# Performance work log

Hardware: AMD Instinct MI355X
Metric: run time of the kernel (lower is better)

Reference implementation:

```python
import jax, jax.numpy as jnp
import numpy as np

NUM_GRAPHS = 256
EPS = 1e-5
SLOPE = 0.01

def _lrelu(x):
    return jnp.where(x >= 0, x, SLOPE * x)

def _gcn(x, W, b, src, dst, ew, n_nodes):
    # GCNConv(normalize=False): out[dst] = sum_e ew[e] * (x @ W)[src[e]] + b
    h = x @ W
    msg = h[src] * ew[:, None]
    agg = jax.ops.segment_sum(msg, dst, num_segments=n_nodes)
    return agg + b

def _bn(x, g, beta):
    # training-mode BatchNorm1d over node dim, biased variance
    m = jnp.mean(x, axis=0)
    v = jnp.mean((x - m) ** 2, axis=0)
    return (x - m) * jax.lax.rsqrt(v + EPS) * g + beta

def setup_inputs() -> dict:
    key = jax.random.key(0)
    ks = jax.random.split(key, 20)
    N, E, F0 = 20000, 320000, 1280
    dims = [(F0, 640), (640, 512), (512, 256), (256, 256)]
    inp = {
        'x': jax.random.normal(ks[0], (N, F0), dtype=jnp.float32),
        'edge_index': jax.random.randint(ks[1], (2, E), 0, N, dtype=jnp.int64),
        'edge_weigth': jax.random.uniform(ks[2], (E,), dtype=jnp.float32),
        'batch': jnp.sort(jax.random.randint(ks[3], (N,), 0, NUM_GRAPHS, dtype=jnp.int64)),
    }
    for i, (fi, fo) in enumerate(dims, start=1):
        inp[f'W{i}'] = jax.random.normal(ks[3 + i], (fi, fo), dtype=jnp.float32) * (1.0 / np.sqrt(fi))
        inp[f'b{i}'] = jnp.zeros((fo,), dtype=jnp.float32)
        inp[f'g{i}'] = jnp.ones((fo,), dtype=jnp.float32)
        inp[f'be{i}'] = jnp.zeros((fo,), dtype=jnp.float32)
    fdims = [(256, 128), (128, 64), (64, 2)]
    for i, (fi, fo) in enumerate(fdims, start=1):
        inp[f'Wf{i}'] = jax.random.normal(ks[10 + i], (fi, fo), dtype=jnp.float32) * np.sqrt(2.0 / (fi + fo))
        inp[f'bf{i}'] = jnp.zeros((fo,), dtype=jnp.float32)
    return inp

def reference(x, edge_index, edge_weigth, batch,
              W1, b1, g1, be1, W2, b2, g2, be2,
              W3, b3, g3, be3, W4, b4, g4, be4,
              Wf1, bf1, Wf2, bf2, Wf3, bf3):
    n = x.shape[0]
    src, dst = edge_index[0], edge_index[1]
    h = _lrelu(_bn(_gcn(x, W1, b1, src, dst, edge_weigth, n), g1, be1))
    h = _lrelu(_bn(_gcn(h, W2, b2, src, dst, edge_weigth, n), g2, be2))
    h = _lrelu(_bn(_gcn(h, W3, b3, src, dst, edge_weigth, n), g3, be3))
    h = _lrelu(_bn(_gcn(h, W4, b4, src, dst, edge_weigth, n), g4, be4))
    pooled = jax.ops.segment_sum(h, batch, num_segments=NUM_GRAPHS)  # [G, 256]
    out = _lrelu(pooled @ Wf1 + bf1)
    out = _lrelu(out @ Wf2 + bf2)
    out = _lrelu(out @ Wf3 + bf3)
    return out
```

## Files before the change

kernel.cpp:

```cpp
#include <hip/hip_runtime.h>

typedef short bf16x8 __attribute__((ext_vector_type(8)));
typedef float f32x4  __attribute__((ext_vector_type(4)));

__device__ __forceinline__ float bf2f(unsigned short h){
  union { unsigned int u; float f; } c; c.u = ((unsigned int)h) << 16; return c.f;
}
__device__ __forceinline__ unsigned short f2bf(float f){
  union { float f; unsigned int u; } c; c.f = f;
  unsigned int u = c.u;
  return (unsigned short)((u + 0x7fffu + ((u >> 16) & 1u)) >> 16);
}
__device__ __forceinline__ void gload_lds16(const void* g, void* l){
  __builtin_amdgcn_global_load_lds((const __attribute__((address_space(1))) unsigned int*)g,
                                   (__attribute__((address_space(3))) unsigned int*)l, 16, 0, 0);
}
__device__ __forceinline__ float lrelu(float x){ return x >= 0.f ? x : 0.01f * x; }

__global__ void cvt_f32_bf16(const float* __restrict__ x, unsigned short* __restrict__ o, int n4){
  int i = blockIdx.x * 256 + threadIdx.x;
  if (i >= n4) return;
  float4 v = ((const float4*)x)[i];
  ushort4 r; r.x = f2bf(v.x); r.y = f2bf(v.y); r.z = f2bf(v.z); r.w = f2bf(v.w);
  ((ushort4*)o)[i] = r;
}

__global__ void wt_kernel(const float* __restrict__ Wm, unsigned short* __restrict__ Wt, int K, int Nf){
  __shared__ float tile[32][33];
  int n0 = blockIdx.x * 32, k0 = blockIdx.y * 32;
  int tx = threadIdx.x, ty = threadIdx.y;
  for (int i = ty; i < 32; i += 8)
    tile[i][tx] = Wm[(size_t)(k0 + i) * Nf + n0 + tx];
  __syncthreads();
  for (int i = ty; i < 32; i += 8)
    Wt[(size_t)(n0 + i) * K + k0 + tx] = f2bf(tile[tx][i]);
}

__global__ void hist_kernel(const int* __restrict__ dst, int* __restrict__ hist, int E){
  int e = blockIdx.x * 256 + threadIdx.x;
  if (e < E) atomicAdd(&hist[dst[e]], 1);
}

__global__ void scan_kernel(int* __restrict__ hist, int* __restrict__ cursor, int n, int total){
  __shared__ int partials[1024];
  const int CH = 20;
  int t = threadIdx.x;
  int base = t * CH;
  int local[CH];
  int s = 0;
  for (int i = 0; i < CH; i++){
    int idx = base + i;
    int v = (idx < n) ? hist[idx] : 0;
    local[i] = s; s += v;
  }
  partials[t] = s;
  __syncthreads();
  for (int off = 1; off < 1024; off <<= 1){
    int v = (t >= off) ? partials[t - off] : 0;
    __syncthreads();
    if (t >= off) partials[t] += v;
    __syncthreads();
  }
  int pre = (t == 0) ? 0 : partials[t - 1];
  for (int i = 0; i < CH; i++){
    int idx = base + i;
    if (idx < n){ int v = pre + local[i]; hist[idx] = v; cursor[idx] = v; }
  }
  if (t == 0){ hist[n] = total; }
}

__global__ void scatter_kernel(const int* __restrict__ src, const int* __restrict__ dst,
                               const float* __restrict__ ew, int* __restrict__ cursor,
                               int* __restrict__ so, float* __restrict__ eo, int E){
  int e = blockIdx.x * 256 + threadIdx.x;
  if (e >= E) return;
  int d = dst[e];
  int p = atomicAdd(&cursor[d], 1);
  so[p] = src[e]; eo[p] = ew[e];
}

__global__ __launch_bounds__(256) void gemm_bf16(const unsigned short* __restrict__ A,
                                                 const unsigned short* __restrict__ Bt,
                                                 unsigned short* __restrict__ C,
                                                 int Nf, int K, int Nt){
  __shared__ unsigned short lsA[128 * 64];
  __shared__ unsigned short lsB[128 * 64];
  const int nwg = gridDim.x;
  const int orig = blockIdx.x;
  const int q = nwg >> 3, r = nwg & 7;
  const int xcd = orig & 7, idx = orig >> 3;
  const int wgid = (xcd < r ? xcd * (q + 1) : r * (q + 1) + (xcd - r) * q) + idx;
  const int mt = wgid / Nt, nt = wgid % Nt;

  const int tid = threadIdx.x;
  const int wave = tid >> 6, lane = tid & 63;
  const int wr = wave >> 1, wc = wave & 1;
  const size_t tm = (size_t)mt * 128, tn = (size_t)nt * 128;

  f32x4 acc[4][4] = {};

  const int lrow = lane >> 3;
  const int lcol = (lane & 7) * 8;
  const unsigned short* Ab = A  + (tm + wave * 32 + lrow) * (size_t)K + lcol;
  const unsigned short* Bb = Bt + (tn + wave * 32 + lrow) * (size_t)K + lcol;
  unsigned short* lA0 = &lsA[(wave * 32) * 64];
  unsigned short* lB0 = &lsB[(wave * 32) * 64];

  for (int k0 = 0; k0 < K; k0 += 64){
    #pragma unroll
    for (int s = 0; s < 4; s++){
      gload_lds16(Ab + (size_t)s * 8 * K + k0, lA0 + s * 8 * 64);
      gload_lds16(Bb + (size_t)s * 8 * K + k0, lB0 + s * 8 * 64);
    }
    __syncthreads();
    #pragma unroll
    for (int kk = 0; kk < 2; kk++){
      bf16x8 af[4], bfr[4];
      #pragma unroll
      for (int m = 0; m < 4; m++)
        af[m] = *(const bf16x8*)&lsA[(wr * 64 + m * 16 + (lane & 15)) * 64 + kk * 32 + (lane >> 4) * 8];
      #pragma unroll
      for (int n = 0; n < 4; n++)
        bfr[n] = *(const bf16x8*)&lsB[(wc * 64 + n * 16 + (lane & 15)) * 64 + kk * 32 + (lane >> 4) * 8];
      #pragma unroll
      for (int m = 0; m < 4; m++)
        #pragma unroll
        for (int n = 0; n < 4; n++)
          acc[m][n] = __builtin_amdgcn_mfma_f32_16x16x32_bf16(af[m], bfr[n], acc[m][n], 0, 0, 0);
    }
    __syncthreads();
  }
  #pragma unroll
  for (int m = 0; m < 4; m++)
    #pragma unroll
    for (int n = 0; n < 4; n++)
      #pragma unroll
      for (int j = 0; j < 4; j++){
        size_t row = tm + wr * 64 + m * 16 + (lane >> 4) * 4 + j;
        size_t col = tn + wc * 64 + n * 16 + (lane & 15);
        C[row * Nf + col] = f2bf(acc[m][n][j]);
      }
}

template<int F, int C, int G, int NPB>
__global__ __launch_bounds__(C * G * NPB)
void agg_panel(const unsigned short* __restrict__ H,
               const int* __restrict__ rp,
               const int* __restrict__ srcs,
               const float* __restrict__ ews,
               float* __restrict__ AGG, int Nnodes){
  const int flat = blockIdx.x;
  const int panel = flat & 7;
  const int ngrp = flat >> 3;
  const int t = threadIdx.x;
  const int c = t % C;
  const int g = (t / C) % G;
  const int ni = t / (C * G);
  const int node = ngrp * NPB + ni;
  const bool valid = (node < Nnodes);
  const size_t coff = (size_t)panel * (C * 8) + (size_t)c * 8;

  int e0 = 0, e1 = 0;
  if (valid){ e0 = rp[node]; e1 = rp[node + 1]; }

  float acc[8] = {0.f,0.f,0.f,0.f,0.f,0.f,0.f,0.f};
  int e = e0 + g;
  for (; e + G < e1; e += 2 * G){
    int s0 = srcs[e];     float w0 = ews[e];
    int s1 = srcs[e + G]; float w1 = ews[e + G];
    bf16x8 v0 = *(const bf16x8*)&H[(size_t)s0 * F + coff];
    bf16x8 v1 = *(const bf16x8*)&H[(size_t)s1 * F + coff];
    #pragma unroll
    for (int j = 0; j < 8; j++) acc[j] += w0 * bf2f((unsigned short)v0[j]);
    #pragma unroll
    for (int j = 0; j < 8; j++) acc[j] += w1 * bf2f((unsigned short)v1[j]);
  }
  if (e < e1){
    int s0 = srcs[e]; float w0 = ews[e];
    bf16x8 v0 = *(const bf16x8*)&H[(size_t)s0 * F + coff];
    #pragma unroll
    for (int j = 0; j < 8; j++) acc[j] += w0 * bf2f((unsigned short)v0[j]);
  }

  __shared__ float red[NPB * G * C * 8];
  if (g > 0){
    #pragma unroll
    for (int j = 0; j < 8; j++) red[((ni * G + g) * C + c) * 8 + j] = acc[j];
  }
  __syncthreads();
  if (g == 0 && valid){
    #pragma unroll
    for (int gg = 1; gg < G; gg++)
      #pragma unroll
      for (int j = 0; j < 8; j++) acc[j] += red[((ni * G + gg) * C + c) * 8 + j];
    float* orow = AGG + (size_t)node * F + coff;
    *(float4*)(orow)     = *(float4*)&acc[0];
    *(float4*)(orow + 4) = *(float4*)&acc[4];
  }
}

__global__ void stats_kernel_v(const float* __restrict__ AGG, float* __restrict__ sum,
                               float* __restrict__ sumsq, int F){
  int nf4 = F >> 2;
  int f4 = blockIdx.x * 256 + threadIdx.x;
  if (f4 >= nf4) return;
  const float4* p = (const float4*)(AGG + (size_t)blockIdx.y * 500 * F) + f4;
  float4 s = {0.f,0.f,0.f,0.f}, q = {0.f,0.f,0.f,0.f};
  for (int r = 0; r < 500; r++){
    float4 v = p[(size_t)r * nf4];
    s.x += v.x; s.y += v.y; s.z += v.z; s.w += v.w;
    q.x += v.x*v.x; q.y += v.y*v.y; q.z += v.z*v.z; q.w += v.w*v.w;
  }
  atomicAdd(&sum[f4*4+0], s.x); atomicAdd(&sum[f4*4+1], s.y);
  atomicAdd(&sum[f4*4+2], s.z); atomicAdd(&sum[f4*4+3], s.w);
  atomicAdd(&sumsq[f4*4+0], q.x); atomicAdd(&sumsq[f4*4+1], q.y);
  atomicAdd(&sumsq[f4*4+2], q.z); atomicAdd(&sumsq[f4*4+3], q.w);
}

__global__ void norm_kernel_v2(const float* __restrict__ AGG, const float* __restrict__ sum,
                               const float* __restrict__ sumsq, const float* __restrict__ gw,
                               const float* __restrict__ bw, unsigned short* __restrict__ OUT,
                               int nf4, int total4){
  int i = blockIdx.x * 256 + threadIdx.x;
  if (i >= total4) return;
  int f4 = i % nf4;
  const float inv = 1.0f / 20000.0f;
  float4 s = ((const float4*)sum)[f4];
  float4 q = ((const float4*)sumsq)[f4];
  float4 g = ((const float4*)gw)[f4];
  float4 b = ((const float4*)bw)[f4];
  float4 a = ((const float4*)AGG)[i];
  ushort4 o;
  { float m = s.x * inv, v = fmaxf(q.x * inv - m * m, 0.f);
    o.x = f2bf(lrelu((a.x - m) * rsqrtf(v + 1e-5f) * g.x + b.x)); }
  { float m = s.y * inv, v = fmaxf(q.y * inv - m * m, 0.f);
    o.y = f2bf(lrelu((a.y - m) * rsqrtf(v + 1e-5f) * g.y + b.y)); }
  { float m = s.z * inv, v = fmaxf(q.z * inv - m * m, 0.f);
    o.z = f2bf(lrelu((a.z - m) * rsqrtf(v + 1e-5f) * g.z + b.z)); }
  { float m = s.w * inv, v = fmaxf(q.w * inv - m * m, 0.f);
    o.w = f2bf(lrelu((a.w - m) * rsqrtf(v + 1e-5f) * g.w + b.w)); }
  ((ushort4*)OUT)[i] = o;
}

__global__ void bounds_kernel(const int* __restrict__ batch, int* __restrict__ gstart, int n){
  int g = threadIdx.x;
  if (g > 256) return;
  int lo = 0, hi = n;
  while (lo < hi){ int mid = (lo + hi) >> 1; if (batch[mid] < g) lo = mid + 1; else hi = mid; }
  gstart[g] = lo;
}

__global__ __launch_bounds__(256) void pool_kernel_v(const unsigned short* __restrict__ A1,
                                                     const int* __restrict__ gstart,
                                                     float* __restrict__ pooled){
  int gph = blockIdx.x;
  int t = threadIdx.x;
  int c = t & 31, g = t >> 5;
  int r0 = gstart[gph], r1 = gstart[gph + 1];
  float acc[8] = {0.f,0.f,0.f,0.f,0.f,0.f,0.f,0.f};
  for (int r = r0 + g; r < r1; r += 8){
    bf16x8 v = *(const bf16x8*)&A1[(size_t)r * 256 + c * 8];
    #pragma unroll
    for (int j = 0; j < 8; j++) acc[j] += bf2f((unsigned short)v[j]);
  }
  __shared__ float red[8][256];
  if (g > 0){
    #pragma unroll
    for (int j = 0; j < 8; j++) red[g][c * 8 + j] = acc[j];
  }
  __syncthreads();
  if (g == 0){
    #pragma unroll
    for (int gg = 1; gg < 8; gg++)
      #pragma unroll
      for (int j = 0; j < 8; j++) acc[j] += red[gg][c * 8 + j];
    #pragma unroll
    for (int j = 0; j < 8; j++) pooled[gph * 256 + c * 8 + j] = acc[j];
  }
}

__global__ void fc_kernel(const float* __restrict__ pooled,
                          const float* __restrict__ Wf1, const float* __restrict__ bf1,
                          const float* __restrict__ Wf2, const float* __restrict__ bf2,
                          const float* __restrict__ Wf3, const float* __restrict__ bf3,
                          float* __restrict__ out){
  int g = blockIdx.x, t = threadIdx.x;
  __shared__ float p0[256], p1[128], p2[64];
  p0[t] = pooled[g * 256 + t];
  p0[t + 128] = pooled[g * 256 + t + 128];
  __syncthreads();
  float a = bf1[t];
  for (int k = 0; k < 256; k++) a += p0[k] * Wf1[k * 128 + t];
  p1[t] = lrelu(a);
  __syncthreads();
  if (t < 64){
    float a2 = bf2[t];
    for (int k = 0; k < 128; k++) a2 += p1[k] * Wf2[k * 64 + t];
    p2[t] = lrelu(a2);
  }
  __syncthreads();
  if (t < 2){
    float a3 = bf3[t];
    for (int k = 0; k < 64; k++) a3 += p2[k] * Wf3[k * 2 + t];
    out[g * 2 + t] = lrelu(a3);
  }
}

extern "C" void kernel_launch(void* const* d_in, const int* in_sizes, int n_in,
                              void* d_out, int out_size, void* d_ws, size_t ws_size,
                              hipStream_t stream){
  const int N = 20000, E = 320000;
  const float* x     = (const float*)d_in[0];
  const int*   ei    = (const int*)d_in[1];
  const float* ew    = (const float*)d_in[2];
  const int*   batch = (const int*)d_in[3];
  const float* W[4]  = {(const float*)d_in[4], (const float*)d_in[8], (const float*)d_in[12], (const float*)d_in[16]};
  const float* gw[4] = {(const float*)d_in[6], (const float*)d_in[10], (const float*)d_in[14], (const float*)d_in[18]};
  const float* bw[4] = {(const float*)d_in[7], (const float*)d_in[11], (const float*)d_in[15], (const float*)d_in[19]};
  const float* Wf1 = (const float*)d_in[20]; const float* bf1 = (const float*)d_in[21];
  const float* Wf2 = (const float*)d_in[22]; const float* bf2 = (const float*)d_in[23];
  const float* Wf3 = (const float*)d_in[24]; const float* bf3 = (const float*)d_in[25];

  const int Kd[4] = {1280, 640, 512, 256};
  const int Nd[4] = {640, 512, 256, 256};

  char* w = (char*)d_ws;
  unsigned short* XB = (unsigned short*)w;
  float* AGG = (float*)w;                 w += 51445760;
  unsigned short* H  = (unsigned short*)w; w += 25722880;
  unsigned short* A1 = (unsigned short*)w; w += 25722880;
  unsigned short* WT = (unsigned short*)w; w += 1638400;
  int*   hist   = (int*)w;   w += 80128;
  int*   cursor = (int*)w;   w += 80128;
  int*   srcs   = (int*)w;   w += 1280000;
  float* ews    = (float*)w; w += 1280000;
  float* sum    = (float*)w; w += 2560;
  float* sumsq  = (float*)w; w += 2560;
  int*   gstart = (int*)w;   w += 1280;
  float* pooled = (float*)w; w += 262144;
  (void)ws_size; (void)n_in; (void)in_sizes; (void)out_size;

  cvt_f32_bf16<<<(N * 1280 / 4 + 255) / 256, 256, 0, stream>>>(x, XB, N * 1280 / 4);

  hipMemsetAsync(hist, 0, 80128, stream);
  hist_kernel<<<E / 256, 256, 0, stream>>>(ei + E, hist, E);
  scan_kernel<<<1, 1024, 0, stream>>>(hist, cursor, N, E);
  scatter_kernel<<<E / 256, 256, 0, stream>>>(ei, ei + E, ew, cursor, srcs, ews, E);

  bounds_kernel<<<1, 320, 0, stream>>>(batch, gstart, N);

  const unsigned short* in = XB;
  for (int l = 0; l < 4; l++){
    int K = Kd[l], Nf = Nd[l];
    int Nt = Nf / 128;
    wt_kernel<<<dim3(Nf / 32, K / 32), dim3(32, 8), 0, stream>>>(W[l], WT, K, Nf);
    gemm_bf16<<<157 * Nt, 256, 0, stream>>>(in, WT, H, Nf, K, Nt);
    if (Nf == 640)      agg_panel<640, 10, 8, 3><<<((N + 2) / 3) * 8, 240, 0, stream>>>(H, hist, srcs, ews, AGG, N);
    else if (Nf == 512) agg_panel<512,  8, 8, 4><<<(N / 4) * 8, 256, 0, stream>>>(H, hist, srcs, ews, AGG, N);
    else                agg_panel<256,  4, 8, 8><<<(N / 8) * 8, 256, 0, stream>>>(H, hist, srcs, ews, AGG, N);
    hipMemsetAsync(sum, 0, 5120, stream);
    stats_kernel_v<<<dim3((Nf / 4 + 255) / 256, 40), 256, 0, stream>>>(AGG, sum, sumsq, Nf);
    int total4 = N * (Nf >> 2);
    norm_kernel_v2<<<(total4 + 255) / 256, 256, 0, stream>>>(AGG, sum, sumsq, gw[l], bw[l], A1, Nf >> 2, total4);
    in = A1;
  }

  pool_kernel_v<<<256, 256, 0, stream>>>(A1, gstart, pooled);
  fc_kernel<<<256, 128, 0, stream>>>(pooled, Wf1, bf1, Wf2, bf2, Wf3, bf3, (float*)d_out);
}
```

Before: 815.3 us.

## Replace panel-split aggregation with one-wavefront-per-node full-row gather

Rewrites the sparse aggregation so each wavefront owns one destination node and gathers entire source rows, instead of splitting the features into 8 panel blocks with edge-group partial sums reduced through shared memory. This removes the LDS reduction, the __syncthreads, and the eightfold repeated reads of CSR indices and weights per node. It also unpacks bf16 pairs with shift/mask and FMA. In exchange, each node's edges are walked serially by one wave, which leaves fewer independent loads in flight per wave, and the 640-wide case uses an uneven split of 16 bytes plus 4 bytes per lane.

```diff
diff --git a/kernel.cpp b/kernel.cpp
--- a/kernel.cpp
+++ b/kernel.cpp
@@ -16,6 +16,11 @@
                                    (__attribute__((address_space(3))) unsigned int*)l, 16, 0, 0);
 }
 __device__ __forceinline__ float lrelu(float x){ return x >= 0.f ? x : 0.01f * x; }
+__device__ __forceinline__ void acc2(float& a0, float& a1, unsigned int u, float w){
+  float lo = __uint_as_float(u << 16);
+  float hi = __uint_as_float(u & 0xffff0000u);
+  a0 = fmaf(lo, w, a0); a1 = fmaf(hi, w, a1);
+}
 
 __global__ void cvt_f32_bf16(const float* __restrict__ x, unsigned short* __restrict__ o, int n4){
   int i = blockIdx.x * 256 + threadIdx.x;
@@ -142,60 +147,61 @@
       }
 }
 
-template<int F, int C, int G, int NPB>
-__global__ __launch_bounds__(C * G * NPB)
-void agg_panel(const unsigned short* __restrict__ H,
-               const int* __restrict__ rp,
-               const int* __restrict__ srcs,
-               const float* __restrict__ ews,
-               float* __restrict__ AGG, int Nnodes){
-  const int flat = blockIdx.x;
-  const int panel = flat & 7;
-  const int ngrp = flat >> 3;
-  const int t = threadIdx.x;
-  const int c = t % C;
-  const int g = (t / C) % G;
-  const int ni = t / (C * G);
-  const int node = ngrp * NPB + ni;
-  const bool valid = (node < Nnodes);
-  const size_t coff = (size_t)panel * (C * 8) + (size_t)c * 8;
-
-  int e0 = 0, e1 = 0;
-  if (valid){ e0 = rp[node]; e1 = rp[node + 1]; }
-
-  float acc[8] = {0.f,0.f,0.f,0.f,0.f,0.f,0.f,0.f};
-  int e = e0 + g;
-  for (; e + G < e1; e += 2 * G){
-    int s0 = srcs[e];     float w0 = ews[e];
-    int s1 = srcs[e + G]; float w1 = ews[e + G];
-    bf16x8 v0 = *(const bf16x8*)&H[(size_t)s0 * F + coff];
-    bf16x8 v1 = *(const bf16x8*)&H[(size_t)s1 * F + coff];
-    #pragma unroll
-    for (int j = 0; j < 8; j++) acc[j] += w0 * bf2f((unsigned short)v0[j]);
-    #pragma unroll
-    for (int j = 0; j < 8; j++) acc[j] += w1 * bf2f((unsigned short)v1[j]);
-  }
-  if (e < e1){
-    int s0 = srcs[e]; float w0 = ews[e];
-    bf16x8 v0 = *(const bf16x8*)&H[(size_t)s0 * F + coff];
-    #pragma unroll
-    for (int j = 0; j < 8; j++) acc[j] += w0 * bf2f((unsigned short)v0[j]);
-  }
-
-  __shared__ float red[NPB * G * C * 8];
-  if (g > 0){
-    #pragma unroll
-    for (int j = 0; j < 8; j++) red[((ni * G + g) * C + c) * 8 + j] = acc[j];
-  }
-  __syncthreads();
-  if (g == 0 && valid){
-    #pragma unroll
-    for (int gg = 1; gg < G; gg++)
-      #pragma unroll
-      for (int j = 0; j < 8; j++) acc[j] += red[((ni * G + gg) * C + c) * 8 + j];
-    float* orow = AGG + (size_t)node * F + coff;
-    *(float4*)(orow)     = *(float4*)&acc[0];
-    *(float4*)(orow + 4) = *(float4*)&acc[4];
+template<int F>
+__global__ __launch_bounds__(256)
+void agg_row(const unsigned short* __restrict__ H,
+             const int* __restrict__ rp,
+             const int* __restrict__ srcs,
+             const float* __restrict__ ews,
+             float* __restrict__ AGG, int Nnodes){
+  const int wv = threadIdx.x >> 6, ln = threadIdx.x & 63;
+  int node = blockIdx.x * 4 + wv;
+  if (node >= Nnodes) return;
+  node = __builtin_amdgcn_readfirstlane(node);
+  const int e0 = rp[node], e1 = rp[node + 1];
+  const unsigned int* Hd = (const unsigned int*)H;
+  constexpr int RD = F / 2;
+
+  float a0=0.f,a1=0.f,a2=0.f,a3=0.f,a4=0.f,a5=0.f,a6=0.f,a7=0.f,a8=0.f,a9=0.f;
+
+  #define AGG_BODY(E) {                                            \
+    int s_ = srcs[E]; float w_ = ews[E];                           \
+    const unsigned int* row_ = Hd + (size_t)s_ * RD;               \
+    if constexpr (F == 256){                                       \
+      uint2 v_ = *(const uint2*)(row_ + ln * 2);                   \
+      acc2(a0,a1,v_.x,w_); acc2(a2,a3,v_.y,w_);                    \
+    } else if constexpr (F == 512){                                \
+      uint4 v_ = *(const uint4*)(row_ + ln * 4);                   \
+      acc2(a0,a1,v_.x,w_); acc2(a2,a3,v_.y,w_);                    \
+      acc2(a4,a5,v_.z,w_); acc2(a6,a7,v_.w,w_);                    \
+    } else {                                                       \
+      uint4 v_ = *(const uint4*)(row_ + ln * 4);                   \
+      unsigned int v2_ = row_[256 + ln];                           \
+      acc2(a0,a1,v_.x,w_); acc2(a2,a3,v_.y,w_);                    \
+      acc2(a4,a5,v_.z,w_); acc2(a6,a7,v_.w,w_);                    \
+      acc2(a8,a9,v2_,w_);                                          \
+    }                                                              \
+  }
+
+  int e = e0;
+  for (; e + 1 < e1; e += 2){ AGG_BODY(e); AGG_BODY(e + 1); }
+  if (e < e1) AGG_BODY(e);
+  #undef AGG_BODY
+
+  float* orow = AGG + (size_t)node * F;
+  if constexpr (F == 256){
+    float4 o = {a0, a1, a2, a3};
+    *(float4*)(orow + ln * 4) = o;
+  } else if constexpr (F == 512){
+    float4 oA = {a0, a1, a2, a3}, oB = {a4, a5, a6, a7};
+    *(float4*)(orow + ln * 8) = oA;
+    *(float4*)(orow + ln * 8 + 4) = oB;
+  } else {
+    float4 oA = {a0, a1, a2, a3}, oB = {a4, a5, a6, a7};
+    *(float4*)(orow + ln * 8) = oA;
+    *(float4*)(orow + ln * 8 + 4) = oB;
+    float2 oC = {a8, a9};
+    *(float2*)(orow + 512 + ln * 2) = oC;
   }
 }
 
@@ -355,9 +361,9 @@
     int Nt = Nf / 128;
     wt_kernel<<<dim3(Nf / 32, K / 32), dim3(32, 8), 0, stream>>>(W[l], WT, K, Nf);
     gemm_bf16<<<157 * Nt, 256, 0, stream>>>(in, WT, H, Nf, K, Nt);
-    if (Nf == 640)      agg_panel<640, 10, 8, 3><<<((N + 2) / 3) * 8, 240, 0, stream>>>(H, hist, srcs, ews, AGG, N);
-    else if (Nf == 512) agg_panel<512,  8, 8, 4><<<(N / 4) * 8, 256, 0, stream>>>(H, hist, srcs, ews, AGG, N);
-    else                agg_panel<256,  4, 8, 8><<<(N / 8) * 8, 256, 0, stream>>>(H, hist, srcs, ews, AGG, N);
+    if (Nf == 640)      agg_row<640><<<(N + 3) / 4, 256, 0, stream>>>(H, hist, srcs, ews, AGG, N);
+    else if (Nf == 512) agg_row<512><<<(N + 3) / 4, 256, 0, stream>>>(H, hist, srcs, ews, AGG, N);
+    else                agg_row<256><<<(N + 3) / 4, 256, 0, stream>>>(H, hist, srcs, ews, AGG, N);
     hipMemsetAsync(sum, 0, 5120, stream);
     stats_kernel_v<<<dim3((Nf / 4 + 255) / 256, 40), 256, 0, stream>>>(AGG, sum, sumsq, Nf);
     int total4 = N * (Nf >> 2);
```

New measurement: 780.9 us. 4.2% less time.
